# Kernel optimization log

Measured on AMD Instinct MI355X. Metric: run time of the kernel, lower is better.

Reference implementation:

```python
import jax, jax.numpy as jnp
import numpy as np

WS = 8        # window_size
NH = 16       # num_heads

def setup_inputs() -> dict:
    key = jax.random.key(0)
    ks = jax.random.split(key, 6)
    B, H, W, C = 16, 64, 64, 512
    nW = (H // WS) * (W // WS)
    return {
        "x": jax.random.normal(ks[0], (B, H * W, C), jnp.float32),
        "qkv_w": jax.random.normal(ks[1], (3 * C, C), jnp.float32) * 0.02,
        "qkv_b": jax.random.normal(ks[2], (3 * C,), jnp.float32) * 0.02,
        "proj_w": jax.random.normal(ks[3], (C, C), jnp.float32) * 0.02,
        "proj_b": jax.random.normal(ks[4], (C,), jnp.float32) * 0.02,
        "attn_mask": jax.random.normal(ks[5], (nW, WS * WS, WS * WS), jnp.float32),
        "H": H,
        "W": W,
    }

def reference(x, qkv_w, qkv_b, proj_w, proj_b, attn_mask, H, W):
    B, N, C = x.shape
    ws = WS
    hd = C // NH
    scale = hd ** (-0.5)
    x_img = x.reshape(B, H, W, C)
    pad_h = (ws - H % ws) % ws
    pad_w = (ws - W % ws) % ws
    if pad_h > 0 or pad_w > 0:
        x_img = jnp.pad(x_img, ((0, 0), (0, pad_h), (0, pad_w), (0, 0)))
    Hp, Wp = H + pad_h, W + pad_w
    nW = (Hp // ws) * (Wp // ws)
    # window partition: [B*nW, ws*ws, C]
    x_win = x_img.reshape(B, Hp // ws, ws, Wp // ws, ws, C)
    x_win = x_win.transpose(0, 1, 3, 2, 4, 5).reshape(B * nW, ws * ws, C)
    # fused qkv projection (torch Linear: y = x @ W^T + b)
    qkv = x_win @ qkv_w.T + qkv_b
    qkv = qkv.reshape(B * nW, ws * ws, 3, NH, hd).transpose(2, 0, 3, 1, 4)
    q, k, v = qkv[0], qkv[1], qkv[2]  # each [B*nW, NH, ws*ws, hd]
    attn = jnp.einsum('bhqd,bhkd->bhqk', q, k) * scale
    if attn_mask is not None:
        attn = attn.reshape(B, nW, NH, ws * ws, ws * ws)
        attn = attn + attn_mask[None, :, None, :, :]
        attn = attn.reshape(B * nW, NH, ws * ws, ws * ws)
    attn = jax.nn.softmax(attn, axis=-1)
    out = jnp.einsum('bhqk,bhkd->bhqd', attn, v)
    out = out.transpose(0, 2, 1, 3).reshape(B * nW, ws * ws, C)
    out = out @ proj_w.T + proj_b
    # window reverse
    out = out.reshape(B, Hp // ws, Wp // ws, ws, ws, C)
    out = out.transpose(0, 1, 3, 2, 4, 5).reshape(B, Hp, Wp, C)
    out = out[:, :H, :W, :].reshape(B, H * W, C)
    return out
```

## Files before the change

### kernel.cpp

```cpp
#include <hip/hip_runtime.h>


typedef unsigned short u16;
typedef unsigned int u32;
typedef __attribute__((ext_vector_type(4))) u16 u16x4;
typedef __attribute__((ext_vector_type(8))) u16 u16x8;
typedef __attribute__((ext_vector_type(8))) short short8;
typedef __attribute__((ext_vector_type(4))) float f32x4;

__device__ __forceinline__ u16 f2bf(float f) {
    u32 u = __float_as_uint(f);
    u += 0x7fffu + ((u >> 16) & 1u);
    return (u16)(u >> 16);
}

__device__ __forceinline__ f32x4 MFMA(u16x8 a, u16x8 b, f32x4 c) {
    return __builtin_amdgcn_mfma_f32_16x16x32_bf16(
        __builtin_bit_cast(short8, a), __builtin_bit_cast(short8, b), c, 0, 0, 0);
}

__device__ __forceinline__ void gload16(const void* g, void* l) {
    __builtin_amdgcn_global_load_lds(
        (const __attribute__((address_space(1))) void*)g,
        (__attribute__((address_space(3))) void*)l, 16, 0, 0);
}

__device__ __forceinline__ int win2img(int r) {
    int b = r >> 12;
    int w = (r >> 6) & 63;
    int t = r & 63;
    int img = (((w >> 3) << 3) + (t >> 3)) * 64 + ((w & 7) << 3) + (t & 7);
    return (b << 12) + img;
}

__device__ __forceinline__ u16x8 cvt8(const float* src) {
    float4 a = *(const float4*)src;
    float4 b = *(const float4*)(src + 4);
    u16x8 t;
    t[0] = f2bf(a.x); t[1] = f2bf(a.y); t[2] = f2bf(a.z); t[3] = f2bf(a.w);
    t[4] = f2bf(b.x); t[5] = f2bf(b.y); t[6] = f2bf(b.z); t[7] = f2bf(b.w);
    return t;
}

__global__ __launch_bounds__(256)
void conv_f2b(const float* __restrict__ in, u16* __restrict__ out, int n8) {
    int u = blockIdx.x * 256 + threadIdx.x;
    if (u >= n8) return;
    *(u16x8*)(out + (size_t)u * 8) = cvt8(in + (size_t)u * 8);
}

__global__ __launch_bounds__(256)
void conv_permute_x(const float* __restrict__ x, u16* __restrict__ xw) {
    int u = blockIdx.x * 256 + threadIdx.x;
    int r = u >> 6;
    int c = (u & 63) << 3;
    int g = win2img(r);
    *(u16x8*)(xw + (size_t)r * 512 + c) = cvt8(x + (size_t)g * 512 + c);
}

__global__ __launch_bounds__(256)
void conv_maskT(const float* __restrict__ mask, float* __restrict__ mT) {
    __shared__ float t[64][65];
    const int w = blockIdx.x;
    const float* mp = mask + ((size_t)w << 12);
    float* op = mT + ((size_t)w << 12);
    const int r = threadIdx.x >> 2, c0 = (threadIdx.x & 3) << 4;
#pragma unroll
    for (int i = 0; i < 4; ++i) {
        float4 v = *(const float4*)(mp + (r << 6) + c0 + i * 4);
        t[c0 + i * 4 + 0][r] = v.x;
        t[c0 + i * 4 + 1][r] = v.y;
        t[c0 + i * 4 + 2][r] = v.z;
        t[c0 + i * 4 + 3][r] = v.w;
    }
    __syncthreads();
#pragma unroll
    for (int i = 0; i < 4; ++i) {
        float4 v;
        v.x = t[r][c0 + i * 4 + 0];
        v.y = t[r][c0 + i * 4 + 1];
        v.z = t[r][c0 + i * 4 + 2];
        v.w = t[r][c0 + i * 4 + 3];
        *(float4*)(op + (r << 6) + c0 + i * 4) = v;
    }
}

#define STAGE(buf, kt) do {                                                   \
    const int ko_ = (kt) * 64;                                                \
    char* d_ = lds + (buf) * 16384 + tb;                                      \
    gload16(aptr + ko_,              d_);                                     \
    gload16(aptr + (64 << 10) + ko_, d_ + 4096);                              \
    gload16(bptr + ko_,              d_ + 8192);                              \
    gload16(bptr + (64 << 10) + ko_, d_ + 12288);                             \
} while (0)

#define COMPUTE(buf) do {                                                     \
    const u16* As_ = (const u16*)(lds + (buf) * 16384);                       \
    const u16* Bs_ = (const u16*)(lds + (buf) * 16384 + 8192);                \
    u16x8 af_[4], bf_[4];                                                     \
    _Pragma("unroll")                                                         \
    for (int mi = 0; mi < 4; ++mi)                                            \
        af_[mi] = *(const u16x8*)(As_ + (wm + mi * 16 + lr) * 32 + lg * 8);   \
    _Pragma("unroll")                                                         \
    for (int ni = 0; ni < 4; ++ni)                                            \
        bf_[ni] = *(const u16x8*)(Bs_ + (wn + ni * 16 + lr) * 32 + lg * 8);   \
    _Pragma("unroll")                                                         \
    for (int mi = 0; mi < 4; ++mi)                                            \
        _Pragma("unroll")                                                     \
        for (int ni = 0; ni < 4; ++ni)                                        \
            acc[mi][ni] = MFMA(af_[mi], bf_[ni], acc[mi][ni]);                \
} while (0)

__global__ __launch_bounds__(256, 4)
void gemm_qkv(const u16* __restrict__ A, const u16* __restrict__ Wt,
              const float* __restrict__ bias, u16* __restrict__ QH,
              u16* __restrict__ KH, u16* __restrict__ VT)
{
    __shared__ char lds[32768];

    const int nwg = gridDim.x;
    const int q   = nwg >> 3;
    const int wg  = ((int)blockIdx.x & 7) * q + ((int)blockIdx.x >> 3);
    const int m0  = (wg / 12) * 128;
    const int n0  = (wg % 12) * 128;

    const int tid  = threadIdx.x;
    const int lane = tid & 63;
    const int wv   = tid >> 6;
    const int wm   = (wv >> 1) << 6;
    const int wn   = (wv & 1) << 6;
    const int lr   = lane & 15;
    const int lg   = lane >> 4;

    const char* aptr = (const char*)A + (((size_t)(m0 + (tid >> 2))) << 10) + ((tid & 3) << 4);
    const char* bptr = (const char*)Wt + (((size_t)(n0 + (tid >> 2))) << 10) + ((tid & 3) << 4);
    const u32 tb = (u32)tid << 4;

    f32x4 acc[4][4] = {};

    STAGE(0, 0);
    __syncthreads();

#pragma unroll 1
    for (int kt = 0; kt < 16; kt += 2) {
        STAGE(1, kt + 1);
        COMPUTE(0);
        __syncthreads();
        if (kt + 2 < 16) STAGE(0, kt + 2);
        COMPUTE(1);
        __syncthreads();
    }

    if (n0 < 1024) {
        u16* __restrict__ P = (n0 < 512) ? QH : KH;
        const int cbase = (n0 < 512) ? n0 : (n0 - 512);
#pragma unroll
        for (int mi = 0; mi < 4; ++mi) {
            const int gr0 = m0 + wm + mi * 16 + lg * 4;
            const int win = gr0 >> 6, ro = gr0 & 63;
#pragma unroll
            for (int ni = 0; ni < 4; ++ni) {
                const int col = cbase + wn + ni * 16 + lr;
                const float bv = bias[(n0 < 512) ? col : (col + 512)];
                const int h = col >> 5, c = col & 31;
                u16* dst = P + (((size_t)win * 16 + h) << 11) + (ro << 5) + c;
#pragma unroll
                for (int r = 0; r < 4; ++r)
                    dst[r << 5] = f2bf(acc[mi][ni][r] + bv);
            }
        }
    } else {
#pragma unroll
        for (int mi = 0; mi < 4; ++mi) {
            const int gr0 = m0 + wm + mi * 16 + lg * 4;
            const int win = gr0 >> 6, ro = gr0 & 63;
#pragma unroll
            for (int ni = 0; ni < 4; ++ni) {
                const int col = n0 + wn + ni * 16 + lr;
                const float bv = bias[col];
                const int d = col - 1024;
                u16x4 h;
#pragma unroll
                for (int r = 0; r < 4; ++r) h[r] = f2bf(acc[mi][ni][r] + bv);
                *(u16x4*)(VT + (((size_t)win << 9) + d) * 64 + ro) = h;
            }
        }
    }
}

__global__ __launch_bounds__(256, 4)
void gemm_proj(const u16* __restrict__ A, const u16* __restrict__ Wt,
               const float* __restrict__ bias, float* __restrict__ C)
{
    __shared__ char lds[32768];

    const int nwg = gridDim.x;
    const int q   = nwg >> 3;
    const int wg  = ((int)blockIdx.x & 7) * q + ((int)blockIdx.x >> 3);
    const int m0  = (wg / 4) * 128;
    const int n0  = (wg % 4) * 128;

    const int tid  = threadIdx.x;
    const int lane = tid & 63;
    const int wv   = tid >> 6;
    const int wm   = (wv >> 1) << 6;
    const int wn   = (wv & 1) << 6;
    const int lr   = lane & 15;
    const int lg   = lane >> 4;

    const char* aptr = (const char*)A + (((size_t)(m0 + (tid >> 2))) << 10) + ((tid & 3) << 4);
    const char* bptr = (const char*)Wt + (((size_t)(n0 + (tid >> 2))) << 10) + ((tid & 3) << 4);
    const u32 tb = (u32)tid << 4;

    f32x4 acc[4][4] = {};

    STAGE(0, 0);
    __syncthreads();

#pragma unroll 1
    for (int kt = 0; kt < 16; kt += 2) {
        STAGE(1, kt + 1);
        COMPUTE(0);
        __syncthreads();
        if (kt + 2 < 16) STAGE(0, kt + 2);
        COMPUTE(1);
        __syncthreads();
    }

#pragma unroll
    for (int mi = 0; mi < 4; ++mi)
#pragma unroll
        for (int ni = 0; ni < 4; ++ni) {
            const int col = n0 + wn + ni * 16 + lr;
            const float bv = bias[col];
#pragma unroll
            for (int r = 0; r < 4; ++r) {
                const int gr = win2img(m0 + wm + mi * 16 + lg * 4 + r);
                C[((size_t)gr << 9) + col] = acc[mi][ni][r] + bv;
            }
        }
}

#undef STAGE
#undef COMPUTE

__global__ __launch_bounds__(256, 3)
void attn_kernel(const u16* __restrict__ QH, const u16* __restrict__ KH,
                 const u16* __restrict__ VT, const float* __restrict__ mT,
                 u16* __restrict__ attn_out)
{
    __shared__ __align__(16) u16 sP[4][64][72];

    const int tid  = threadIdx.x;
    const int lane = tid & 63;
    const int wv   = tid >> 6;
    const int lr   = lane & 15;
    const int lg   = lane >> 4;
    const int win  = blockIdx.x;
    const int wib  = win & 63;
    const size_t rb = (size_t)win << 6;
    const float* mtp = mT + ((size_t)wib << 12);
    const u16* qbase = QH + ((size_t)win << 15);
    const u16* kbase = KH + ((size_t)win << 15);
    const u16* vbase = VT + ((size_t)win << 15);
    const float scale = 0.17677669529663687f;

#pragma unroll 1
    for (int hi = 0; hi < 4; ++hi) {
        const int h = hi * 4 + wv;
        const int hoff = h * 32;
        const u16* qh = qbase + (h << 11);
        const u16* kh = kbase + (h << 11);

        u16x8 qf[4], kf[4];
#pragma unroll
        for (int mt = 0; mt < 4; ++mt) {
            const int off = ((mt * 16 + lr) << 5) + (lg << 3);
            qf[mt] = *(const u16x8*)(qh + off);
            kf[mt] = *(const u16x8*)(kh + off);
        }
        f32x4 s[4][4] = {};
#pragma unroll
        for (int mi = 0; mi < 4; ++mi)
#pragma unroll
            for (int ni = 0; ni < 4; ++ni)
                s[mi][ni] = MFMA(qf[mi], kf[ni], s[mi][ni]);

        float rsum[4][4];
#pragma unroll
        for (int mi = 0; mi < 4; ++mi) {
            float4 mv[4];
#pragma unroll
            for (int ni = 0; ni < 4; ++ni)
                mv[ni] = *(const float4*)(mtp + (ni * 16 + lr) * 64 + mi * 16 + lg * 4);
#pragma unroll
            for (int r = 0; r < 4; ++r) {
                float vv[4];
                float mx = -1e30f;
#pragma unroll
                for (int ni = 0; ni < 4; ++ni) {
                    float v = s[mi][ni][r] * scale + ((const float*)&mv[ni])[r];
                    vv[ni] = v;
                    mx = fmaxf(mx, v);
                }
#pragma unroll
                for (int mk = 1; mk <= 8; mk <<= 1)
                    mx = fmaxf(mx, __shfl_xor(mx, mk, 64));
                float sum = 0.f;
#pragma unroll
                for (int ni = 0; ni < 4; ++ni) {
                    float p = __expf(vv[ni] - mx);
                    sum += p;
                    s[mi][ni][r] = p;
                }
#pragma unroll
                for (int mk = 1; mk <= 8; mk <<= 1)
                    sum += __shfl_xor(sum, mk, 64);
                rsum[mi][r] = sum;
            }
        }

        __syncthreads();
#pragma unroll
        for (int mi = 0; mi < 4; ++mi)
#pragma unroll
            for (int ni = 0; ni < 4; ++ni)
#pragma unroll
                for (int r = 0; r < 4; ++r)
                    sP[wv][mi * 16 + lg * 4 + r][ni * 16 + lr] = f2bf(s[mi][ni][r]);
        __syncthreads();

        u16x8 pf[4][2];
#pragma unroll
        for (int mt = 0; mt < 4; ++mt)
#pragma unroll
            for (int k2 = 0; k2 < 2; ++k2)
                pf[mt][k2] = *(const u16x8*)&sP[wv][mt * 16 + lr][k2 * 32 + lg * 8];

        u16x8 vf[2][2];
#pragma unroll
        for (int k2 = 0; k2 < 2; ++k2)
#pragma unroll
            for (int nt = 0; nt < 2; ++nt)
                vf[k2][nt] = *(const u16x8*)(vbase
                    + ((size_t)(hoff + nt * 16 + lr) << 6) + k2 * 32 + lg * 8);

        f32x4 o[4][2] = {};
#pragma unroll
        for (int mt = 0; mt < 4; ++mt)
#pragma unroll
            for (int k2 = 0; k2 < 2; ++k2)
#pragma unroll
                for (int nt = 0; nt < 2; ++nt)
                    o[mt][nt] = MFMA(pf[mt][k2], vf[k2][nt], o[mt][nt]);

#pragma unroll
        for (int mt = 0; mt < 4; ++mt)
#pragma unroll
            for (int nt = 0; nt < 2; ++nt)
#pragma unroll
                for (int r = 0; r < 4; ++r) {
                    const int row = mt * 16 + lg * 4 + r;
                    const int d = nt * 16 + lr;
                    attn_out[((rb + row) << 9) + hoff + d] =
                        f2bf(o[mt][nt][r] / rsum[mt][r]);
                }
    }
}

extern "C" void kernel_launch(void* const* d_in, const int* in_sizes, int n_in,
                              void* d_out, int out_size, void* d_ws, size_t ws_size,
                              hipStream_t stream)
{
    const float* x      = (const float*)d_in[0];
    const float* qkv_w  = (const float*)d_in[1];
    const float* qkv_b  = (const float*)d_in[2];
    const float* proj_w = (const float*)d_in[3];
    const float* proj_b = (const float*)d_in[4];
    const float* mask   = (const float*)d_in[5];
    float* out = (float*)d_out;

    const size_t WQKV  = 1536ull * 512;
    const size_t WPROJ = 512ull * 512;
    const size_t MTSZ  = 64ull * 64 * 64;

    u16* wq = (u16*)d_ws;
    u16* wp = wq + WQKV;
    float* mTg = (float*)(wp + WPROJ);
    u16* chunk = (u16*)(mTg + MTSZ);

    const size_t xwPB  = 4096ull * 512;
    const size_t qhPB  = 4096ull * 512;
    const size_t khPB  = 4096ull * 512;
    const size_t vtPB  = 4096ull * 512;
    const size_t attPB = 4096ull * 512;
    const size_t perBatchBytes = (xwPB + qhPB + khPB + vtPB + attPB) * 2;

    size_t avail = ws_size - (WQKV + WPROJ) * 2 - MTSZ * 4;
    int Bc = (int)(avail / perBatchBytes);
    if (Bc > 16) Bc = 16;
    if (Bc < 1) Bc = 1;

    u16* xw_ws  = chunk;
    u16* qh_ws  = xw_ws + (size_t)Bc * xwPB;
    u16* kh_ws  = qh_ws + (size_t)Bc * qhPB;
    u16* vt_ws  = kh_ws + (size_t)Bc * khPB;
    u16* att_ws = vt_ws + (size_t)Bc * vtPB;

    conv_f2b<<<dim3((WQKV / 8 + 255) / 256), 256, 0, stream>>>(qkv_w, wq, (int)(WQKV / 8));
    conv_f2b<<<dim3((WPROJ / 8 + 255) / 256), 256, 0, stream>>>(proj_w, wp, (int)(WPROJ / 8));
    conv_maskT<<<dim3(64), 256, 0, stream>>>(mask, mTg);

    for (int b0 = 0; b0 < 16; b0 += Bc) {
        const int bc = (16 - b0) < Bc ? (16 - b0) : Bc;
        const float* xc = x + (size_t)b0 * 4096 * 512;
        float* outc = out + (size_t)b0 * 4096 * 512;

        conv_permute_x<<<dim3(bc * 1024), 256, 0, stream>>>(xc, xw_ws);
        gemm_qkv<<<dim3(bc * 32 * 12), 256, 0, stream>>>(
            xw_ws, wq, qkv_b, qh_ws, kh_ws, vt_ws);
        attn_kernel<<<dim3(bc * 64), 256, 0, stream>>>(
            qh_ws, kh_ws, vt_ws, mTg, att_ws);
        gemm_proj<<<dim3(bc * 32 * 4), 256, 0, stream>>>(
            att_ws, wp, proj_b, outc);
    }
}
```

Before: 338.9 us.

## Fuse window attention with output projection in one per-window kernel

Merges attn_kernel and gemm_proj into one 512-thread kernel. Each workgroup handles one window, computes all 16 heads with 8 waves, stages the bf16 attention output in LDS, then multiplies it by the projection weight read straight from global memory without LDS staging. This removes the intermediate attention buffer's global write and read and one launch per chunk, and frees workspace so more batches fit per chunk. The cost is heavy LDS use (about 140 KB) limiting occupancy to one workgroup per CU. The projection weight is reloaded from global/L2 by every window, and the old pipelined LDS-tiled GEMM is gone.

```diff
diff --git a/kernel.cpp b/kernel.cpp
--- a/kernel.cpp
+++ b/kernel.cpp
@@ -188,68 +188,17 @@
     }
 }
 
-__global__ __launch_bounds__(256, 4)
-void gemm_proj(const u16* __restrict__ A, const u16* __restrict__ Wt,
-               const float* __restrict__ bias, float* __restrict__ C)
-{
-    __shared__ char lds[32768];
-
-    const int nwg = gridDim.x;
-    const int q   = nwg >> 3;
-    const int wg  = ((int)blockIdx.x & 7) * q + ((int)blockIdx.x >> 3);
-    const int m0  = (wg / 4) * 128;
-    const int n0  = (wg % 4) * 128;
-
-    const int tid  = threadIdx.x;
-    const int lane = tid & 63;
-    const int wv   = tid >> 6;
-    const int wm   = (wv >> 1) << 6;
-    const int wn   = (wv & 1) << 6;
-    const int lr   = lane & 15;
-    const int lg   = lane >> 4;
-
-    const char* aptr = (const char*)A + (((size_t)(m0 + (tid >> 2))) << 10) + ((tid & 3) << 4);
-    const char* bptr = (const char*)Wt + (((size_t)(n0 + (tid >> 2))) << 10) + ((tid & 3) << 4);
-    const u32 tb = (u32)tid << 4;
-
-    f32x4 acc[4][4] = {};
-
-    STAGE(0, 0);
-    __syncthreads();
-
-#pragma unroll 1
-    for (int kt = 0; kt < 16; kt += 2) {
-        STAGE(1, kt + 1);
-        COMPUTE(0);
-        __syncthreads();
-        if (kt + 2 < 16) STAGE(0, kt + 2);
-        COMPUTE(1);
-        __syncthreads();
-    }
-
-#pragma unroll
-    for (int mi = 0; mi < 4; ++mi)
-#pragma unroll
-        for (int ni = 0; ni < 4; ++ni) {
-            const int col = n0 + wn + ni * 16 + lr;
-            const float bv = bias[col];
-#pragma unroll
-            for (int r = 0; r < 4; ++r) {
-                const int gr = win2img(m0 + wm + mi * 16 + lg * 4 + r);
-                C[((size_t)gr << 9) + col] = acc[mi][ni][r] + bv;
-            }
-        }
-}
-
 #undef STAGE
 #undef COMPUTE
 
-__global__ __launch_bounds__(256, 3)
-void attn_kernel(const u16* __restrict__ QH, const u16* __restrict__ KH,
-                 const u16* __restrict__ VT, const float* __restrict__ mT,
-                 u16* __restrict__ attn_out)
+__global__ __launch_bounds__(512, 1)
+void attn_proj(const u16* __restrict__ QH, const u16* __restrict__ KH,
+               const u16* __restrict__ VT, const float* __restrict__ mT,
+               const u16* __restrict__ Wp, const float* __restrict__ pbias,
+               float* __restrict__ out)
 {
-    __shared__ __align__(16) u16 sP[4][64][72];
+    __shared__ __align__(16) u16 sP[8][64][72];
+    __shared__ __align__(16) u16 sO[64][520];
 
     const int tid  = threadIdx.x;
     const int lane = tid & 63;
@@ -258,16 +207,15 @@
     const int lg   = lane >> 4;
     const int win  = blockIdx.x;
     const int wib  = win & 63;
-    const size_t rb = (size_t)win << 6;
     const float* mtp = mT + ((size_t)wib << 12);
     const u16* qbase = QH + ((size_t)win << 15);
     const u16* kbase = KH + ((size_t)win << 15);
     const u16* vbase = VT + ((size_t)win << 15);
     const float scale = 0.17677669529663687f;
 
-#pragma unroll 1
-    for (int hi = 0; hi < 4; ++hi) {
-        const int h = hi * 4 + wv;
+#pragma unroll
+    for (int hi = 0; hi < 2; ++hi) {
+        const int h = hi * 8 + wv;
         const int hoff = h * 32;
         const u16* qh = qbase + (h << 11);
         const u16* kh = kbase + (h << 11);
@@ -320,7 +268,6 @@
             }
         }
 
-        __syncthreads();
 #pragma unroll
         for (int mi = 0; mi < 4; ++mi)
 #pragma unroll
@@ -328,7 +275,6 @@
 #pragma unroll
                 for (int r = 0; r < 4; ++r)
                     sP[wv][mi * 16 + lg * 4 + r][ni * 16 + lr] = f2bf(s[mi][ni][r]);
-        __syncthreads();
 
         u16x8 pf[4][2];
 #pragma unroll
@@ -359,12 +305,44 @@
 #pragma unroll
             for (int nt = 0; nt < 2; ++nt)
 #pragma unroll
-                for (int r = 0; r < 4; ++r) {
-                    const int row = mt * 16 + lg * 4 + r;
-                    const int d = nt * 16 + lr;
-                    attn_out[((rb + row) << 9) + hoff + d] =
+                for (int r = 0; r < 4; ++r)
+                    sO[mt * 16 + lg * 4 + r][hoff + nt * 16 + lr] =
                         f2bf(o[mt][nt][r] / rsum[mt][r]);
-                }
+    }
+
+    __syncthreads();
+
+    f32x4 acc[4][4] = {};
+    const u16* wrow = Wp + ((size_t)(wv * 64 + lr) << 9) + (lg << 3);
+
+#pragma unroll 2
+    for (int ks = 0; ks < 16; ++ks) {
+        u16x8 af[4], bf[4];
+#pragma unroll
+        for (int mi = 0; mi < 4; ++mi)
+            af[mi] = *(const u16x8*)&sO[mi * 16 + lr][ks * 32 + lg * 8];
+#pragma unroll
+        for (int ni = 0; ni < 4; ++ni)
+            bf[ni] = *(const u16x8*)(wrow + ((size_t)(ni * 16) << 9) + ks * 32);
+#pragma unroll
+        for (int mi = 0; mi < 4; ++mi)
+#pragma unroll
+            for (int ni = 0; ni < 4; ++ni)
+                acc[mi][ni] = MFMA(af[mi], bf[ni], acc[mi][ni]);
+    }
+
+#pragma unroll
+    for (int ni = 0; ni < 4; ++ni) {
+        const int col = wv * 64 + ni * 16 + lr;
+        const float bv = pbias[col];
+#pragma unroll
+        for (int mi = 0; mi < 4; ++mi) {
+#pragma unroll
+            for (int r = 0; r < 4; ++r) {
+                const int gr = win2img((win << 6) + mi * 16 + lg * 4 + r);
+                out[((size_t)gr << 9) + col] = acc[mi][ni][r] + bv;
+            }
+        }
     }
 }
 
@@ -393,8 +371,7 @@
     const size_t qhPB  = 4096ull * 512;
     const size_t khPB  = 4096ull * 512;
     const size_t vtPB  = 4096ull * 512;
-    const size_t attPB = 4096ull * 512;
-    const size_t perBatchBytes = (xwPB + qhPB + khPB + vtPB + attPB) * 2;
+    const size_t perBatchBytes = (xwPB + qhPB + khPB + vtPB) * 2;
 
     size_t avail = ws_size - (WQKV + WPROJ) * 2 - MTSZ * 4;
     int Bc = (int)(avail / perBatchBytes);
@@ -405,7 +382,6 @@
     u16* qh_ws  = xw_ws + (size_t)Bc * xwPB;
     u16* kh_ws  = qh_ws + (size_t)Bc * qhPB;
     u16* vt_ws  = kh_ws + (size_t)Bc * khPB;
-    u16* att_ws = vt_ws + (size_t)Bc * vtPB;
 
     conv_f2b<<<dim3((WQKV / 8 + 255) / 256), 256, 0, stream>>>(qkv_w, wq, (int)(WQKV / 8));
     conv_f2b<<<dim3((WPROJ / 8 + 255) / 256), 256, 0, stream>>>(proj_w, wp, (int)(WPROJ / 8));
@@ -419,9 +395,7 @@
         conv_permute_x<<<dim3(bc * 1024), 256, 0, stream>>>(xc, xw_ws);
         gemm_qkv<<<dim3(bc * 32 * 12), 256, 0, stream>>>(
             xw_ws, wq, qkv_b, qh_ws, kh_ws, vt_ws);
-        attn_kernel<<<dim3(bc * 64), 256, 0, stream>>>(
-            qh_ws, kh_ws, vt_ws, mTg, att_ws);
-        gemm_proj<<<dim3(bc * 32 * 4), 256, 0, stream>>>(
-            att_ws, wp, proj_b, outc);
-    }
-}
+        attn_proj<<<dim3(bc * 64), 512, 0, stream>>>(
+            qh_ws, kh_ws, vt_ws, mTg, wp, proj_b, outc);
+    }
+}
```

Result: slower. 376.1 us (+11.0%).

## Fuse x window-permute and bf16 conversion into QKV GEMM; simplify softmax

Applied to the files above, without the earlier changes.

Drops the separate conv_permute_x pass: the QKV GEMM now pulls fp32 rows of x straight from image order into LDS through a swizzled layout and converts them to bf16 while building MFMA fragments. This removes the bf16 x workspace and one full read and write of x. The softmax scale and log2e are folded into Q and the mask so softmax becomes a bare exp2. The max subtraction and two block barriers are gone, which risks overflow if the logits get large. The fp32 A tile doubles LDS use, so occupancy is lowered to 3 workgroups.

```diff
diff --git a/kernel.cpp b/kernel.cpp
--- a/kernel.cpp
+++ b/kernel.cpp
@@ -6,7 +6,11 @@
 typedef __attribute__((ext_vector_type(4))) u16 u16x4;
 typedef __attribute__((ext_vector_type(8))) u16 u16x8;
 typedef __attribute__((ext_vector_type(8))) short short8;
+typedef __attribute__((ext_vector_type(8))) __bf16 bf16x8;
 typedef __attribute__((ext_vector_type(4))) float f32x4;
+
+#define QSCALE 0.2550301122936858f
+#define LOG2E  1.4426950408889634f
 
 __device__ __forceinline__ u16 f2bf(float f) {
     u32 u = __float_as_uint(f);
@@ -50,15 +54,6 @@
 }
 
 __global__ __launch_bounds__(256)
-void conv_permute_x(const float* __restrict__ x, u16* __restrict__ xw) {
-    int u = blockIdx.x * 256 + threadIdx.x;
-    int r = u >> 6;
-    int c = (u & 63) << 3;
-    int g = win2img(r);
-    *(u16x8*)(xw + (size_t)r * 512 + c) = cvt8(x + (size_t)g * 512 + c);
-}
-
-__global__ __launch_bounds__(256)
 void conv_maskT(const float* __restrict__ mask, float* __restrict__ mT) {
     __shared__ float t[64][65];
     const int w = blockIdx.x;
@@ -68,10 +63,10 @@
 #pragma unroll
     for (int i = 0; i < 4; ++i) {
         float4 v = *(const float4*)(mp + (r << 6) + c0 + i * 4);
-        t[c0 + i * 4 + 0][r] = v.x;
-        t[c0 + i * 4 + 1][r] = v.y;
-        t[c0 + i * 4 + 2][r] = v.z;
-        t[c0 + i * 4 + 3][r] = v.w;
+        t[c0 + i * 4 + 0][r] = v.x * LOG2E;
+        t[c0 + i * 4 + 1][r] = v.y * LOG2E;
+        t[c0 + i * 4 + 2][r] = v.z * LOG2E;
+        t[c0 + i * 4 + 3][r] = v.w * LOG2E;
     }
     __syncthreads();
 #pragma unroll
@@ -85,38 +80,13 @@
     }
 }
 
-#define STAGE(buf, kt) do {                                                   \
-    const int ko_ = (kt) * 64;                                                \
-    char* d_ = lds + (buf) * 16384 + tb;                                      \
-    gload16(aptr + ko_,              d_);                                     \
-    gload16(aptr + (64 << 10) + ko_, d_ + 4096);                              \
-    gload16(bptr + ko_,              d_ + 8192);                              \
-    gload16(bptr + (64 << 10) + ko_, d_ + 12288);                             \
-} while (0)
-
-#define COMPUTE(buf) do {                                                     \
-    const u16* As_ = (const u16*)(lds + (buf) * 16384);                       \
-    const u16* Bs_ = (const u16*)(lds + (buf) * 16384 + 8192);                \
-    u16x8 af_[4], bf_[4];                                                     \
-    _Pragma("unroll")                                                         \
-    for (int mi = 0; mi < 4; ++mi)                                            \
-        af_[mi] = *(const u16x8*)(As_ + (wm + mi * 16 + lr) * 32 + lg * 8);   \
-    _Pragma("unroll")                                                         \
-    for (int ni = 0; ni < 4; ++ni)                                            \
-        bf_[ni] = *(const u16x8*)(Bs_ + (wn + ni * 16 + lr) * 32 + lg * 8);   \
-    _Pragma("unroll")                                                         \
-    for (int mi = 0; mi < 4; ++mi)                                            \
-        _Pragma("unroll")                                                     \
-        for (int ni = 0; ni < 4; ++ni)                                        \
-            acc[mi][ni] = MFMA(af_[mi], bf_[ni], acc[mi][ni]);                \
-} while (0)
-
-__global__ __launch_bounds__(256, 4)
-void gemm_qkv(const u16* __restrict__ A, const u16* __restrict__ Wt,
+__global__ __launch_bounds__(256, 3)
+void gemm_qkv(const float* __restrict__ X, const u16* __restrict__ Wt,
               const float* __restrict__ bias, u16* __restrict__ QH,
               u16* __restrict__ KH, u16* __restrict__ VT)
 {
-    __shared__ char lds[32768];
+    __shared__ float sA[2][128 * 32];
+    __shared__ u16   sB[2][128 * 32];
 
     const int nwg = gridDim.x;
     const int q   = nwg >> 3;
@@ -132,11 +102,56 @@
     const int lr   = lane & 15;
     const int lg   = lane >> 4;
 
-    const char* aptr = (const char*)A + (((size_t)(m0 + (tid >> 2))) << 10) + ((tid & 3) << 4);
+    const int srow = tid >> 3;
+    const int gu   = (tid & 7) ^ (srow & 7);
+    const float* ap0 = X + ((size_t)win2img(m0 + srow)      << 9) + gu * 4;
+    const float* ap1 = X + ((size_t)win2img(m0 + 32 + srow) << 9) + gu * 4;
+    const float* ap2 = X + ((size_t)win2img(m0 + 64 + srow) << 9) + gu * 4;
+    const float* ap3 = X + ((size_t)win2img(m0 + 96 + srow) << 9) + gu * 4;
+
     const char* bptr = (const char*)Wt + (((size_t)(n0 + (tid >> 2))) << 10) + ((tid & 3) << 4);
-    const u32 tb = (u32)tid << 4;
+
+    const int xu1 = (((lg << 1)      ^ (lr & 7)) << 2);
+    const int xu2 = ((((lg << 1) | 1) ^ (lr & 7)) << 2);
 
     f32x4 acc[4][4] = {};
+
+#define STAGE(buf, kt) do {                                                   \
+    char* dA_ = (char*)&sA[buf][0] + tid * 16;                                \
+    gload16(ap0 + (kt) * 32, dA_);                                            \
+    gload16(ap1 + (kt) * 32, dA_ + 4096);                                     \
+    gload16(ap2 + (kt) * 32, dA_ + 8192);                                     \
+    gload16(ap3 + (kt) * 32, dA_ + 12288);                                    \
+    char* dB_ = (char*)&sB[buf][0] + tid * 16;                                \
+    gload16(bptr + (kt) * 64, dB_);                                           \
+    gload16(bptr + (64 << 10) + (kt) * 64, dB_ + 4096);                       \
+} while (0)
+
+#define COMPUTE(buf) do {                                                     \
+    const float* As_ = &sA[buf][0];                                           \
+    const u16*   Bs_ = &sB[buf][0];                                           \
+    u16x8 af_[4], bf_[4];                                                     \
+    _Pragma("unroll")                                                         \
+    for (int mi = 0; mi < 4; ++mi) {                                          \
+        const float* rp_ = As_ + (wm + mi * 16 + lr) * 32;                    \
+        float4 fa_ = *(const float4*)(rp_ + xu1);                             \
+        float4 fb_ = *(const float4*)(rp_ + xu2);                             \
+        bf16x8 t_;                                                            \
+        t_[0] = (__bf16)fa_.x; t_[1] = (__bf16)fa_.y;                         \
+        t_[2] = (__bf16)fa_.z; t_[3] = (__bf16)fa_.w;                         \
+        t_[4] = (__bf16)fb_.x; t_[5] = (__bf16)fb_.y;                         \
+        t_[6] = (__bf16)fb_.z; t_[7] = (__bf16)fb_.w;                         \
+        af_[mi] = __builtin_bit_cast(u16x8, t_);                              \
+    }                                                                         \
+    _Pragma("unroll")                                                         \
+    for (int ni = 0; ni < 4; ++ni)                                            \
+        bf_[ni] = *(const u16x8*)(Bs_ + (wn + ni * 16 + lr) * 32 + lg * 8);   \
+    _Pragma("unroll")                                                         \
+    for (int mi = 0; mi < 4; ++mi)                                            \
+        _Pragma("unroll")                                                     \
+        for (int ni = 0; ni < 4; ++ni)                                        \
+            acc[mi][ni] = MFMA(af_[mi], bf_[ni], acc[mi][ni]);                \
+} while (0)
 
     STAGE(0, 0);
     __syncthreads();
@@ -151,9 +166,13 @@
         __syncthreads();
     }
 
+#undef STAGE
+#undef COMPUTE
+
     if (n0 < 1024) {
         u16* __restrict__ P = (n0 < 512) ? QH : KH;
         const int cbase = (n0 < 512) ? n0 : (n0 - 512);
+        const float fs = (n0 < 512) ? QSCALE : 1.0f;
 #pragma unroll
         for (int mi = 0; mi < 4; ++mi) {
             const int gr0 = m0 + wm + mi * 16 + lg * 4;
@@ -166,7 +185,7 @@
                 u16* dst = P + (((size_t)win * 16 + h) << 11) + (ro << 5) + c;
 #pragma unroll
                 for (int r = 0; r < 4; ++r)
-                    dst[r << 5] = f2bf(acc[mi][ni][r] + bv);
+                    dst[r << 5] = f2bf((acc[mi][ni][r] + bv) * fs);
             }
         }
     } else {
@@ -214,18 +233,47 @@
 
     f32x4 acc[4][4] = {};
 
-    STAGE(0, 0);
+#define PSTG(buf, kt) do {                                                    \
+    const int ko_ = (kt) * 64;                                                \
+    char* d_ = lds + (buf) * 16384 + tb;                                      \
+    gload16(aptr + ko_,              d_);                                     \
+    gload16(aptr + (64 << 10) + ko_, d_ + 4096);                              \
+    gload16(bptr + ko_,              d_ + 8192);                              \
+    gload16(bptr + (64 << 10) + ko_, d_ + 12288);                             \
+} while (0)
+
+#define PCMP(buf) do {                                                        \
+    const u16* As_ = (const u16*)(lds + (buf) * 16384);                       \
+    const u16* Bs_ = (const u16*)(lds + (buf) * 16384 + 8192);                \
+    u16x8 af_[4], bf_[4];                                                     \
+    _Pragma("unroll")                                                         \
+    for (int mi = 0; mi < 4; ++mi)                                            \
+        af_[mi] = *(const u16x8*)(As_ + (wm + mi * 16 + lr) * 32 + lg * 8);   \
+    _Pragma("unroll")                                                         \
+    for (int ni = 0; ni < 4; ++ni)                                            \
+        bf_[ni] = *(const u16x8*)(Bs_ + (wn + ni * 16 + lr) * 32 + lg * 8);   \
+    _Pragma("unroll")                                                         \
+    for (int mi = 0; mi < 4; ++mi)                                            \
+        _Pragma("unroll")                                                     \
+        for (int ni = 0; ni < 4; ++ni)                                        \
+            acc[mi][ni] = MFMA(af_[mi], bf_[ni], acc[mi][ni]);                \
+} while (0)
+
+    PSTG(0, 0);
     __syncthreads();
 
 #pragma unroll 1
     for (int kt = 0; kt < 16; kt += 2) {
-        STAGE(1, kt + 1);
-        COMPUTE(0);
+        PSTG(1, kt + 1);
+        PCMP(0);
         __syncthreads();
-        if (kt + 2 < 16) STAGE(0, kt + 2);
-        COMPUTE(1);
+        if (kt + 2 < 16) PSTG(0, kt + 2);
+        PCMP(1);
         __syncthreads();
     }
+
+#undef PSTG
+#undef PCMP
 
 #pragma unroll
     for (int mi = 0; mi < 4; ++mi)
@@ -240,9 +288,6 @@
             }
         }
 }
-
-#undef STAGE
-#undef COMPUTE
 
 __global__ __launch_bounds__(256, 3)
 void attn_kernel(const u16* __restrict__ QH, const u16* __restrict__ KH,
@@ -263,7 +308,6 @@
     const u16* qbase = QH + ((size_t)win << 15);
     const u16* kbase = KH + ((size_t)win << 15);
     const u16* vbase = VT + ((size_t)win << 15);
-    const float scale = 0.17677669529663687f;
 
 #pragma unroll 1
     for (int hi = 0; hi < 4; ++hi) {
@@ -295,21 +339,10 @@
                 mv[ni] = *(const float4*)(mtp + (ni * 16 + lr) * 64 + mi * 16 + lg * 4);
 #pragma unroll
             for (int r = 0; r < 4; ++r) {
-                float vv[4];
-                float mx = -1e30f;
+                float sum = 0.f;
 #pragma unroll
                 for (int ni = 0; ni < 4; ++ni) {
-                    float v = s[mi][ni][r] * scale + ((const float*)&mv[ni])[r];
-                    vv[ni] = v;
-                    mx = fmaxf(mx, v);
-                }
-#pragma unroll
-                for (int mk = 1; mk <= 8; mk <<= 1)
-                    mx = fmaxf(mx, __shfl_xor(mx, mk, 64));
-                float sum = 0.f;
-#pragma unroll
-                for (int ni = 0; ni < 4; ++ni) {
-                    float p = __expf(vv[ni] - mx);
+                    float p = exp2f(s[mi][ni][r] + ((const float*)&mv[ni])[r]);
                     sum += p;
                     s[mi][ni][r] = p;
                 }
@@ -320,7 +353,6 @@
             }
         }
 
-        __syncthreads();
 #pragma unroll
         for (int mi = 0; mi < 4; ++mi)
 #pragma unroll
@@ -328,7 +360,6 @@
 #pragma unroll
                 for (int r = 0; r < 4; ++r)
                     sP[wv][mi * 16 + lg * 4 + r][ni * 16 + lr] = f2bf(s[mi][ni][r]);
-        __syncthreads();
 
         u16x8 pf[4][2];
 #pragma unroll
@@ -389,20 +420,18 @@
     float* mTg = (float*)(wp + WPROJ);
     u16* chunk = (u16*)(mTg + MTSZ);
 
-    const size_t xwPB  = 4096ull * 512;
     const size_t qhPB  = 4096ull * 512;
     const size_t khPB  = 4096ull * 512;
     const size_t vtPB  = 4096ull * 512;
     const size_t attPB = 4096ull * 512;
-    const size_t perBatchBytes = (xwPB + qhPB + khPB + vtPB + attPB) * 2;
+    const size_t perBatchBytes = (qhPB + khPB + vtPB + attPB) * 2;
 
     size_t avail = ws_size - (WQKV + WPROJ) * 2 - MTSZ * 4;
     int Bc = (int)(avail / perBatchBytes);
     if (Bc > 16) Bc = 16;
     if (Bc < 1) Bc = 1;
 
-    u16* xw_ws  = chunk;
-    u16* qh_ws  = xw_ws + (size_t)Bc * xwPB;
+    u16* qh_ws  = chunk;
     u16* kh_ws  = qh_ws + (size_t)Bc * qhPB;
     u16* vt_ws  = kh_ws + (size_t)Bc * khPB;
     u16* att_ws = vt_ws + (size_t)Bc * vtPB;
@@ -416,9 +445,8 @@
         const float* xc = x + (size_t)b0 * 4096 * 512;
         float* outc = out + (size_t)b0 * 4096 * 512;
 
-        conv_permute_x<<<dim3(bc * 1024), 256, 0, stream>>>(xc, xw_ws);
         gemm_qkv<<<dim3(bc * 32 * 12), 256, 0, stream>>>(
-            xw_ws, wq, qkv_b, qh_ws, kh_ws, vt_ws);
+            xc, wq, qkv_b, qh_ws, kh_ws, vt_ws);
         attn_kernel<<<dim3(bc * 64), 256, 0, stream>>>(
             qh_ws, kh_ws, vt_ws, mTg, att_ws);
         gemm_proj<<<dim3(bc * 32 * 4), 256, 0, stream>>>(
```

Result: slower. 362.4 us (+6.9%).
